# Kernel optimization log

Measured on AMD Instinct MI355X. Metric: run time of the kernel, lower is better.

The kernel has to match this reference:

```python
import jax, jax.numpy as jnp
import numpy as np
import math

IN_CH = 256
CH = 128
SCALE = math.sqrt(CH)
TEMPERATURE = 1.0


def setup_inputs() -> dict:
    key = jax.random.key(0)
    ks = jax.random.split(key, 9)
    B, C, H, W = 8, IN_CH, 56, 56
    x = jax.random.normal(ks[0], (B, C, H, W), dtype=jnp.float32)
    s_in = 1.0 / math.sqrt(IN_CH)
    s_ch = 1.0 / math.sqrt(CH)
    wq = jax.random.uniform(ks[1], (CH, IN_CH), minval=-s_in, maxval=s_in)
    bq = jax.random.uniform(ks[2], (CH,), minval=-s_in, maxval=s_in)
    wk = jax.random.uniform(ks[3], (CH, IN_CH), minval=-s_in, maxval=s_in)
    bk = jax.random.uniform(ks[4], (CH,), minval=-s_in, maxval=s_in)
    wv = jax.random.uniform(ks[5], (CH, IN_CH), minval=-s_in, maxval=s_in)
    bv = jax.random.uniform(ks[6], (CH,), minval=-s_in, maxval=s_in)
    wo = jax.random.uniform(ks[7], (IN_CH, CH), minval=-s_ch, maxval=s_ch)
    bo = jax.random.uniform(ks[8], (IN_CH,), minval=-s_ch, maxval=s_ch)
    return {"x": x, "wq": wq, "bq": bq, "wk": wk, "bk": bk,
            "wv": wv, "bv": bv, "wo": wo, "bo": bo}


def reference(x, wq, bq, wk, bk, wv, bv, wo, bo):
    B, C, H, W = x.shape
    N = H * W
    xf = x.reshape(B, C, N)  # flatten spatial; 1x1 conv == channel matmul
    q = jnp.einsum('oc,bcn->bon', wq, xf) + bq[None, :, None]  # (B,CH,N)
    k = jnp.einsum('oc,bcn->bon', wk, xf) + bk[None, :, None]
    v = jnp.einsum('oc,bcn->bon', wv, xf) + bv[None, :, None]
    # similarity map (B, N, N): query positions x key positions
    sim = jnp.einsum('bcn,bcm->bnm', q, k) / (SCALE * TEMPERATURE)
    attn = jax.nn.softmax(sim, axis=2)
    out = jnp.einsum('bnm,bcm->bnc', attn, v)  # (B, N, CH)
    out = jnp.einsum('oc,bnc->bon', wo, out) + bo[None, :, None]  # (B,IN_CH,N)
    return x + out.reshape(B, C, H, W)
```

## Files before the change

kernel.cpp:

```cpp
#include <hip/hip_runtime.h>
#include <hip/hip_bf16.h>
#include <math.h>

#define NPOS 3136
#define NB   8
#define LOG2E 1.44269504088896f
#define QSCALE (0.08838834764831845f * LOG2E)
#define OFS2  11.54156032711168f

typedef __attribute__((ext_vector_type(8))) short shortx8;
typedef __attribute__((ext_vector_type(4))) short shortx4;
typedef __attribute__((ext_vector_type(4))) float f32x4;
typedef __attribute__((ext_vector_type(16))) float f32x16;
typedef __attribute__((ext_vector_type(4))) unsigned int uint4v;

struct S8pair { shortx4 lo, hi; };

__device__ __forceinline__ float bf2f(unsigned short u) {
    unsigned int i = ((unsigned int)u) << 16;
    return __builtin_bit_cast(float, i);
}
__device__ __forceinline__ unsigned short f2bf(float f) {
    unsigned int i = __builtin_bit_cast(unsigned int, f);
    i += 0x7FFFu + ((i >> 16) & 1u);
    return (unsigned short)(i >> 16);
}
__device__ __forceinline__ void gll16(const unsigned short* g, unsigned short* l) {
    __builtin_amdgcn_global_load_lds((const __attribute__((address_space(1))) void*)g,
                                     (__attribute__((address_space(3))) void*)l, 16, 0, 0);
}

__global__ __launch_bounds__(256) void cast_w(
    const float* __restrict__ wq, const float* __restrict__ wk,
    const float* __restrict__ wv, const float* __restrict__ wo,
    unsigned short* __restrict__ Wb)
{
    const int sel = blockIdx.y;
    const float* src = (sel == 0) ? wq : (sel == 1) ? wk : (sel == 2) ? wv : wo;
    const float sc = (sel == 0) ? QSCALE : 1.0f;
    unsigned short* dst = Wb + sel * 32768;
    int i0 = (blockIdx.x * 256 + threadIdx.x) * 8;
    #pragma unroll
    for (int e = 0; e < 8; ++e) dst[i0 + e] = f2bf(src[i0 + e] * sc);
}

__global__ __launch_bounds__(256) void cast_xT(
    const float* __restrict__ x, unsigned short* __restrict__ xT)
{
    const int b = blockIdx.z, c0 = blockIdx.y * 64, n0 = blockIdx.x * 64;
    __shared__ unsigned short Ls[64 * 66];
    const int t = threadIdx.x;
    {
        int r = t >> 2, q4 = t & 3;
        const float* src = x + ((size_t)b * 256 + c0 + r) * NPOS + n0 + q4 * 16;
        #pragma unroll
        for (int i = 0; i < 16; ++i) Ls[r * 66 + q4 * 16 + i] = f2bf(src[i]);
    }
    __syncthreads();
    {
        int j = t >> 2, h4 = t & 3;
        shortx8 v0, v1;
        #pragma unroll
        for (int i = 0; i < 8; ++i) v0[i] = (short)Ls[(h4 * 16 + i) * 66 + j];
        #pragma unroll
        for (int i = 0; i < 8; ++i) v1[i] = (short)Ls[(h4 * 16 + 8 + i) * 66 + j];
        unsigned short* dst = xT + ((size_t)b * NPOS + n0 + j) * 256 + c0 + h4 * 16;
        *reinterpret_cast<shortx8*>(dst) = v0;
        *reinterpret_cast<shortx8*>(dst + 8) = v1;
    }
}

__global__ __launch_bounds__(256) void qkv_mfma(
    const unsigned short* __restrict__ xT,
    const unsigned short* __restrict__ Wb,
    const float* __restrict__ bq, const float* __restrict__ bk, const float* __restrict__ bv,
    unsigned short* __restrict__ qT, unsigned short* __restrict__ kT,
    unsigned short* __restrict__ vC)
{
    const int b = blockIdx.z, sel = blockIdx.y, n0 = blockIdx.x * 64;
    const int t = threadIdx.x, lane = t & 63, wave = t >> 6;
    const int l16 = lane & 15, lhi = lane >> 4;
    __shared__ __align__(16) unsigned short Wt[128 * 128];
    __shared__ __align__(16) unsigned short Xt[64 * 128];
    const unsigned short* Wsel = Wb + sel * 32768;
    const float* bias = (sel == 0) ? bq : (sel == 1) ? bk : bv;

    f32x4 acc[2][4];
    #pragma unroll
    for (int ab = 0; ab < 2; ++ab)
        #pragma unroll
        for (int nb = 0; nb < 4; ++nb) acc[ab][nb] = f32x4{0.f, 0.f, 0.f, 0.f};

    for (int ks0 = 0; ks0 < 2; ++ks0) {
        const int k0 = ks0 * 128;
        __syncthreads();
        #pragma unroll
        for (int i = 0; i < 8; ++i) {
            int c = (wave * 8 + i) * 64 + lane;
            int row = c >> 4, cin = (c & 15) ^ (row & 7);
            gll16(Wsel + (size_t)row * 256 + k0 + cin * 8, &Wt[0] + (wave * 8 + i) * 512);
        }
        #pragma unroll
        for (int i = 0; i < 4; ++i) {
            int c = (wave * 4 + i) * 64 + lane;
            int row = c >> 4, cin = (c & 15) ^ (row & 7);
            gll16(xT + ((size_t)b * NPOS + n0 + row) * 256 + k0 + cin * 8,
                  &Xt[0] + (wave * 4 + i) * 512);
        }
        __syncthreads();
        #pragma unroll
        for (int ks = 0; ks < 4; ++ks) {
            shortx8 aW[2];
            #pragma unroll
            for (int ab = 0; ab < 2; ++ab) {
                int row = wave * 32 + ab * 16 + l16;
                int idx = (row * 128 + ks * 32 + lhi * 8) ^ ((row & 7) << 3);
                aW[ab] = *reinterpret_cast<const shortx8*>(Wt + idx);
            }
            #pragma unroll
            for (int nb = 0; nb < 4; ++nb) {
                int row = nb * 16 + l16;
                int idx = (row * 128 + ks * 32 + lhi * 8) ^ ((row & 7) << 3);
                shortx8 bX = *reinterpret_cast<const shortx8*>(Xt + idx);
                acc[0][nb] = __builtin_amdgcn_mfma_f32_16x16x32_bf16(aW[0], bX, acc[0][nb], 0, 0, 0);
                acc[1][nb] = __builtin_amdgcn_mfma_f32_16x16x32_bf16(aW[1], bX, acc[1][nb], 0, 0, 0);
            }
        }
    }
    const int strip = wave * 32;
    if (sel < 2) {
        unsigned short* dst0 = ((sel == 0) ? qT : kT) + (size_t)b * NPOS * 128;
        const float bsc = (sel == 0) ? QSCALE : 1.0f;
        #pragma unroll
        for (int ab = 0; ab < 2; ++ab) {
            int ocb = strip + ab * 16 + lhi * 4;
            float bb[4];
            #pragma unroll
            for (int j = 0; j < 4; ++j) bb[j] = bias[ocb + j] * bsc;
            #pragma unroll
            for (int nb = 0; nb < 4; ++nb) {
                int n = n0 + nb * 16 + l16;
                shortx4 u;
                #pragma unroll
                for (int j = 0; j < 4; ++j) u[j] = (short)f2bf(acc[ab][nb][j] + bb[j]);
                *reinterpret_cast<shortx4*>(dst0 + (size_t)n * 128 + ocb) = u;
            }
        }
    } else {
        #pragma unroll
        for (int ab = 0; ab < 2; ++ab)
            #pragma unroll
            for (int j = 0; j < 4; ++j) {
                int oc = strip + ab * 16 + lhi * 4 + j;
                float bb = bias[oc];
                unsigned short* dst = vC + ((size_t)b * 128 + oc) * NPOS + n0;
                #pragma unroll
                for (int nb = 0; nb < 4; ++nb)
                    dst[nb * 16 + l16] = f2bf(acc[ab][nb][j] + bb);
            }
    }
}

__global__ __launch_bounds__(256) void attn_kernel(
    const unsigned short* __restrict__ qT,
    const unsigned short* __restrict__ kT,
    const unsigned short* __restrict__ vC,
    unsigned short* __restrict__ ao,
    float* __restrict__ lrG)
{
    const int i_lin = blockIdx.y * 49 + blockIdx.x;
    const int b = i_lin & 7;
    const int n0 = (i_lin >> 3) * 64;
    const int t = threadIdx.x, lane = t & 63, wave = t >> 6;
    const int l31 = lane & 31, h = lane >> 5;
    const int qsub = wave >> 1, kh = wave & 1;
    const int NT = NPOS / 64;

    __shared__ __align__(16) unsigned short KsB[2][64 * 128];
    __shared__ __align__(16) unsigned short VsB[2][128 * 64];

    shortx8 aQ[8];
    {
        const unsigned short* qp = qT + ((size_t)b * NPOS + n0 + qsub * 32 + l31) * 128 + h * 8;
        #pragma unroll
        for (int kk = 0; kk < 8; ++kk)
            aQ[kk] = *reinterpret_cast<const shortx8*>(qp + kk * 16);
    }

    const unsigned short* kSrc[4];
    const unsigned short* vSrc[4];
    unsigned sDst[4];
    #pragma unroll
    for (int i = 0; i < 4; ++i) {
        int c = (wave * 4 + i) * 64 + lane;
        int rK = c >> 4, cK = (c & 15) ^ (rK & 15);
        kSrc[i] = kT + ((size_t)b * NPOS + rK) * 128 + cK * 8;
        int rV = c >> 3, cV = (c & 7) ^ (rV & 7);
        vSrc[i] = vC + ((size_t)b * 128 + rV) * NPOS + cV * 8;
        sDst[i] = (wave * 4 + i) * 512;
    }

    unsigned kIdx[8];
    {
        int rowK = kh * 32 + l31;
        #pragma unroll
        for (int kk = 0; kk < 8; ++kk)
            kIdx[kk] = rowK * 128 + (((kk * 2 + h) ^ (rowK & 15)) * 8);
    }
    unsigned vBase[4], vM8[4];
    #pragma unroll
    for (int ob = 0; ob < 4; ++ob) {
        int rowV = ob * 32 + l31;
        vBase[ob] = rowV * 64 + h * 4;
        vM8[ob] = (rowV & 7) * 8;
    }

    f32x16 o[4];
    #pragma unroll
    for (int ob = 0; ob < 4; ++ob)
        #pragma unroll
        for (int r = 0; r < 16; ++r) o[ob][r] = 0.f;
    float lrP = 0.f;

    #define STAGE(kt_, buf_)                                                          \
        _Pragma("unroll")                                                             \
        for (int i = 0; i < 4; ++i) {                                                 \
            gll16(kSrc[i] + (size_t)(kt_) * 8192, &KsB[buf_][0] + sDst[i]);           \
            gll16(vSrc[i] + (kt_) * 64, &VsB[buf_][0] + sDst[i]);                     \
        }

    #define COMPUTE(Ks, Vs)                                                           \
    {                                                                                 \
        f32x16 sA, sB;                                                                \
        _Pragma("unroll")                                                             \
        for (int r = 0; r < 16; ++r) { sA[r] = 0.f; sB[r] = 0.f; }                    \
        __builtin_amdgcn_s_setprio(1);                                                \
        _Pragma("unroll")                                                             \
        for (int kk = 0; kk < 8; kk += 2) {                                           \
            shortx8 k0 = *reinterpret_cast<const shortx8*>((Ks) + kIdx[kk]);          \
            shortx8 k1 = *reinterpret_cast<const shortx8*>((Ks) + kIdx[kk + 1]);      \
            sA = __builtin_amdgcn_mfma_f32_32x32x16_bf16(k0, aQ[kk], sA, 0, 0, 0);    \
            sB = __builtin_amdgcn_mfma_f32_32x32x16_bf16(k1, aQ[kk + 1], sB, 0, 0, 0);\
        }                                                                             \
        __builtin_amdgcn_s_setprio(0);                                                \
        unsigned pk[8];                                                               \
        _Pragma("unroll")                                                             \
        for (int g = 0; g < 4; ++g) {                                                 \
            float p0 = exp2f(sA[g * 4 + 0] + sB[g * 4 + 0] - OFS2);                   \
            float p1 = exp2f(sA[g * 4 + 1] + sB[g * 4 + 1] - OFS2);                   \
            float p2 = exp2f(sA[g * 4 + 2] + sB[g * 4 + 2] - OFS2);                   \
            float p3 = exp2f(sA[g * 4 + 3] + sB[g * 4 + 3] - OFS2);                   \
            lrP += (p0 + p1) + (p2 + p3);                                             \
            asm("v_cvt_pk_bf16_f32 %0, %1, %2" : "=v"(pk[g * 2 + 0]) : "v"(p0), "v"(p1)); \
            asm("v_cvt_pk_bf16_f32 %0, %1, %2" : "=v"(pk[g * 2 + 1]) : "v"(p2), "v"(p3)); \
        }                                                                             \
        __builtin_amdgcn_s_setprio(1);                                                \
        _Pragma("unroll")                                                             \
        for (int ks = 0; ks < 2; ++ks) {                                              \
            uint4v pv = {pk[ks * 4 + 0], pk[ks * 4 + 1], pk[ks * 4 + 2], pk[ks * 4 + 3]}; \
            shortx8 PA = __builtin_bit_cast(shortx8, pv);                             \
            _Pragma("unroll")                                                         \
            for (int ob = 0; ob < 4; ++ob) {                                          \
                unsigned i0 = vBase[ob] + (((kh * 4 + ks * 2 + 0) * 8) ^ vM8[ob]);    \
                unsigned i1 = vBase[ob] + (((kh * 4 + ks * 2 + 1) * 8) ^ vM8[ob]);    \
                shortx4 lo = *reinterpret_cast<const shortx4*>((Vs) + i0);            \
                shortx4 hi = *reinterpret_cast<const shortx4*>((Vs) + i1);            \
                shortx8 bV = __builtin_bit_cast(shortx8, S8pair{lo, hi});             \
                o[ob] = __builtin_amdgcn_mfma_f32_32x32x16_bf16(PA, bV, o[ob], 0, 0, 0); \
            }                                                                         \
        }                                                                             \
        __builtin_amdgcn_s_setprio(0);                                                \
    }

    STAGE(0, 0)
    STAGE(1, 1)

    int cur = 0;
    for (int kt = 0; kt < NT - 1; ++kt) {
        asm volatile("s_waitcnt vmcnt(8)" ::: "memory");
        __builtin_amdgcn_sched_barrier(0);
        __builtin_amdgcn_s_barrier();
        __builtin_amdgcn_sched_barrier(0);
        COMPUTE(&KsB[cur][0], &VsB[cur][0])
        __builtin_amdgcn_sched_barrier(0);
        __builtin_amdgcn_s_barrier();
        __builtin_amdgcn_sched_barrier(0);
        if (kt < NT - 2) { STAGE(kt + 2, cur) }
        cur ^= 1;
    }
    {
        asm volatile("s_waitcnt vmcnt(0)" ::: "memory");
        __builtin_amdgcn_sched_barrier(0);
        __builtin_amdgcn_s_barrier();
        COMPUTE(&KsB[cur][0], &VsB[cur][0])
    }
    __syncthreads();

    float lr2 = lrP + __shfl_xor(lrP, 32);
    float* Om = reinterpret_cast<float*>(&KsB[0][0]);
    float* lrS = reinterpret_cast<float*>(&VsB[1][0]);
    unsigned short* Oo = &VsB[0][0];

    if (kh == 1) {
        #pragma unroll
        for (int ob = 0; ob < 4; ++ob)
            #pragma unroll
            for (int r = 0; r < 16; ++r) {
                int q = qsub * 32 + (r & 3) + 8 * (r >> 2) + 4 * h;
                Om[q * 128 + ob * 32 + l31] = o[ob][r];
            }
        if (lane < 32) lrS[qsub * 32 + l31] = lr2;
    }
    __syncthreads();
    if (kh == 0) {
        #pragma unroll
        for (int ob = 0; ob < 4; ++ob)
            #pragma unroll
            for (int r = 0; r < 16; ++r) {
                int q = qsub * 32 + (r & 3) + 8 * (r >> 2) + 4 * h;
                int idx = q * 128 + ob * 32 + l31;
                Oo[idx] = f2bf(o[ob][r] + Om[idx]);
            }
        if (lane < 32)
            lrG[(size_t)b * NPOS + n0 + qsub * 32 + l31] = lr2 + lrS[qsub * 32 + l31];
    }
    __syncthreads();
    {
        const shortx8* src = reinterpret_cast<const shortx8*>(Oo);
        shortx8* dst = reinterpret_cast<shortx8*>(ao + ((size_t)b * NPOS + n0) * 128);
        #pragma unroll
        for (int i = 0; i < 4; ++i) dst[t + 256 * i] = src[t + 256 * i];
    }
    #undef STAGE
    #undef COMPUTE
}

__global__ __launch_bounds__(256) void out_proj(
    const float* __restrict__ x,
    const unsigned short* __restrict__ Wb,
    const float* __restrict__ bo,
    const unsigned short* __restrict__ ao,
    const float* __restrict__ lrG,
    float* __restrict__ y)
{
    const int b = blockIdx.y, n0 = blockIdx.x * 64;
    const int t = threadIdx.x, lane = t & 63, wave = t >> 6;
    const int l16 = lane & 15, lhi = lane >> 4;
    __shared__ __align__(16) unsigned short Wt[256 * 128];
    __shared__ __align__(16) unsigned short At[64 * 128];
    const unsigned short* wo = Wb + 98304;

    #pragma unroll
    for (int i = 0; i < 16; ++i) {
        int c = (wave * 16 + i) * 64 + lane;
        int row = c >> 4, cin = (c & 15) ^ (row & 7);
        gll16(wo + (size_t)row * 128 + cin * 8, &Wt[0] + (wave * 16 + i) * 512);
    }
    #pragma unroll
    for (int i = 0; i < 4; ++i) {
        int c = (wave * 4 + i) * 64 + lane;
        int row = c >> 4, cin = (c & 15) ^ (row & 7);
        gll16(ao + ((size_t)b * NPOS + n0 + row) * 128 + cin * 8, &At[0] + (wave * 4 + i) * 512);
    }
    __syncthreads();

    f32x4 acc[4][4];
    #pragma unroll
    for (int ab = 0; ab < 4; ++ab)
        #pragma unroll
        for (int nb = 0; nb < 4; ++nb) acc[ab][nb] = f32x4{0.f, 0.f, 0.f, 0.f};

    const int strip = wave * 64;
    #pragma unroll
    for (int ks = 0; ks < 4; ++ks) {
        shortx8 aW[4];
        #pragma unroll
        for (int ab = 0; ab < 4; ++ab) {
            int row = strip + ab * 16 + l16;
            int idx = (row * 128 + ks * 32 + lhi * 8) ^ ((row & 7) << 3);
            aW[ab] = *reinterpret_cast<const shortx8*>(Wt + idx);
        }
        #pragma unroll
        for (int nb = 0; nb < 4; ++nb) {
            int row = nb * 16 + l16;
            int idx = (row * 128 + ks * 32 + lhi * 8) ^ ((row & 7) << 3);
            shortx8 bA = *reinterpret_cast<const shortx8*>(At + idx);
            #pragma unroll
            for (int ab = 0; ab < 4; ++ab)
                acc[ab][nb] = __builtin_amdgcn_mfma_f32_16x16x32_bf16(aW[ab], bA, acc[ab][nb], 0, 0, 0);
        }
    }

    float inv[4];
    #pragma unroll
    for (int nb = 0; nb < 4; ++nb)
        inv[nb] = 1.0f / lrG[(size_t)b * NPOS + n0 + nb * 16 + l16];

    #pragma unroll
    for (int ab = 0; ab < 4; ++ab)
        #pragma unroll
        for (int j = 0; j < 4; ++j) {
            int oc = strip + ab * 16 + lhi * 4 + j;
            float bb = bo[oc];
            const float* xr = x + ((size_t)b * 256 + oc) * NPOS + n0;
            float* yr = y + ((size_t)b * 256 + oc) * NPOS + n0;
            #pragma unroll
            for (int nb = 0; nb < 4; ++nb) {
                int n = nb * 16 + l16;
                yr[n] = xr[n] + bb + acc[ab][nb][j] * inv[nb];
            }
        }
}

extern "C" void kernel_launch(void* const* d_in, const int* in_sizes, int n_in,
                              void* d_out, int out_size, void* d_ws, size_t ws_size,
                              hipStream_t stream)
{
    const float* x  = (const float*)d_in[0];
    const float* wq = (const float*)d_in[1];
    const float* bq = (const float*)d_in[2];
    const float* wk = (const float*)d_in[3];
    const float* bk = (const float*)d_in[4];
    const float* wv = (const float*)d_in[5];
    const float* bv = (const float*)d_in[6];
    const float* wo = (const float*)d_in[7];
    const float* bo = (const float*)d_in[8];
    float* y = (float*)d_out;

    const size_t sz = (size_t)NB * NPOS * 128;
    unsigned short* qT = (unsigned short*)d_ws;
    unsigned short* kT = qT + sz;
    unsigned short* vC = kT + sz;
    unsigned short* xT = vC + sz;
    unsigned short* ao = xT;
    unsigned short* Wb = xT + 2 * sz;
    float* lrG = (float*)(Wb + 131072);

    cast_w  <<<dim3(16, 4),       256, 0, stream>>>(wq, wk, wv, wo, Wb);
    cast_xT <<<dim3(49, 4, NB),   256, 0, stream>>>(x, xT);
    qkv_mfma<<<dim3(49, 3, NB),   256, 0, stream>>>(xT, Wb, bq, bk, bv, qT, kT, vC);
    attn_kernel<<<dim3(49, NB),   256, 0, stream>>>(qT, kT, vC, ao, lrG);
    out_proj<<<dim3(49, NB),      256, 0, stream>>>(x, Wb, bo, ao, lrG, y);
}
```

Measured before the change: 122.2 us.

## Split attention key range across two blocks and merge partials in out_proj

The attention kernel now launches twice as many blocks, and each one covers half of the 49 key tiles (25 and 24). Each block writes an unnormalized partial output and a partial row sum to separate slices of the workspace, which the output projection sums before dividing. The aim is to fill the GPU's compute units better, since 392 blocks on 256 CUs leaves the machine unevenly loaded, and 784 smaller blocks balance it. The cost is extra traffic for the partial outputs and double the A-operand loads and MFMAs in out_proj. It relies on the fixed exponent offset rather than a running max, so the partials can be added without rescaling. V LDS indices are also precomputed into registers.

```diff
diff --git a/kernel.cpp b/kernel.cpp
--- a/kernel.cpp
+++ b/kernel.cpp
@@ -168,13 +168,15 @@
     unsigned short* __restrict__ ao,
     float* __restrict__ lrG)
 {
-    const int i_lin = blockIdx.y * 49 + blockIdx.x;
-    const int b = i_lin & 7;
-    const int n0 = (i_lin >> 3) * 64;
+    const int id = blockIdx.x + 49 * blockIdx.y + 392 * blockIdx.z;
+    const int b = id & 7;
+    const int r = id >> 3;
+    const int z = (r >= 49) ? 1 : 0;
+    const int n0 = (z ? r - 49 : r) * 64;
+    const int kt0 = z ? 25 : 0, kt1 = z ? 49 : 25;
     const int t = threadIdx.x, lane = t & 63, wave = t >> 6;
     const int l31 = lane & 31, h = lane >> 5;
     const int qsub = wave >> 1, kh = wave & 1;
-    const int NT = NPOS / 64;
 
     __shared__ __align__(16) unsigned short KsB[2][64 * 128];
     __shared__ __align__(16) unsigned short VsB[2][128 * 64];
@@ -207,19 +209,23 @@
         for (int kk = 0; kk < 8; ++kk)
             kIdx[kk] = rowK * 128 + (((kk * 2 + h) ^ (rowK & 15)) * 8);
     }
-    unsigned vBase[4], vM8[4];
+    unsigned vIdx[4][2][2];
     #pragma unroll
     for (int ob = 0; ob < 4; ++ob) {
         int rowV = ob * 32 + l31;
-        vBase[ob] = rowV * 64 + h * 4;
-        vM8[ob] = (rowV & 7) * 8;
+        #pragma unroll
+        for (int ks = 0; ks < 2; ++ks)
+            #pragma unroll
+            for (int rr = 0; rr < 2; ++rr)
+                vIdx[ob][ks][rr] = rowV * 64 + h * 4
+                    + (((kh * 4 + ks * 2 + rr) * 8) ^ ((rowV & 7) * 8));
     }
 
     f32x16 o[4];
     #pragma unroll
     for (int ob = 0; ob < 4; ++ob)
         #pragma unroll
-        for (int r = 0; r < 16; ++r) o[ob][r] = 0.f;
+        for (int r2 = 0; r2 < 16; ++r2) o[ob][r2] = 0.f;
     float lrP = 0.f;
 
     #define STAGE(kt_, buf_)                                                          \
@@ -233,7 +239,7 @@
     {                                                                                 \
         f32x16 sA, sB;                                                                \
         _Pragma("unroll")                                                             \
-        for (int r = 0; r < 16; ++r) { sA[r] = 0.f; sB[r] = 0.f; }                    \
+        for (int r2 = 0; r2 < 16; ++r2) { sA[r2] = 0.f; sB[r2] = 0.f; }               \
         __builtin_amdgcn_s_setprio(1);                                                \
         _Pragma("unroll")                                                             \
         for (int kk = 0; kk < 8; kk += 2) {                                           \
@@ -261,10 +267,8 @@
             shortx8 PA = __builtin_bit_cast(shortx8, pv);                             \
             _Pragma("unroll")                                                         \
             for (int ob = 0; ob < 4; ++ob) {                                          \
-                unsigned i0 = vBase[ob] + (((kh * 4 + ks * 2 + 0) * 8) ^ vM8[ob]);    \
-                unsigned i1 = vBase[ob] + (((kh * 4 + ks * 2 + 1) * 8) ^ vM8[ob]);    \
-                shortx4 lo = *reinterpret_cast<const shortx4*>((Vs) + i0);            \
-                shortx4 hi = *reinterpret_cast<const shortx4*>((Vs) + i1);            \
+                shortx4 lo = *reinterpret_cast<const shortx4*>((Vs) + vIdx[ob][ks][0]); \
+                shortx4 hi = *reinterpret_cast<const shortx4*>((Vs) + vIdx[ob][ks][1]); \
                 shortx8 bV = __builtin_bit_cast(shortx8, S8pair{lo, hi});             \
                 o[ob] = __builtin_amdgcn_mfma_f32_32x32x16_bf16(PA, bV, o[ob], 0, 0, 0); \
             }                                                                         \
@@ -272,11 +276,11 @@
         __builtin_amdgcn_s_setprio(0);                                                \
     }
 
-    STAGE(0, 0)
-    STAGE(1, 1)
+    STAGE(kt0, 0)
+    STAGE(kt0 + 1, 1)
 
     int cur = 0;
-    for (int kt = 0; kt < NT - 1; ++kt) {
+    for (int kt = kt0; kt < kt1 - 1; ++kt) {
         asm volatile("s_waitcnt vmcnt(8)" ::: "memory");
         __builtin_amdgcn_sched_barrier(0);
         __builtin_amdgcn_s_barrier();
@@ -285,7 +289,7 @@
         __builtin_amdgcn_sched_barrier(0);
         __builtin_amdgcn_s_barrier();
         __builtin_amdgcn_sched_barrier(0);
-        if (kt < NT - 2) { STAGE(kt + 2, cur) }
+        if (kt < kt1 - 2) { STAGE(kt + 2, cur) }
         cur ^= 1;
     }
     {
@@ -305,9 +309,9 @@
         #pragma unroll
         for (int ob = 0; ob < 4; ++ob)
             #pragma unroll
-            for (int r = 0; r < 16; ++r) {
-                int q = qsub * 32 + (r & 3) + 8 * (r >> 2) + 4 * h;
-                Om[q * 128 + ob * 32 + l31] = o[ob][r];
+            for (int r2 = 0; r2 < 16; ++r2) {
+                int q = qsub * 32 + (r2 & 3) + 8 * (r2 >> 2) + 4 * h;
+                Om[q * 128 + ob * 32 + l31] = o[ob][r2];
             }
         if (lane < 32) lrS[qsub * 32 + l31] = lr2;
     }
@@ -316,18 +320,20 @@
         #pragma unroll
         for (int ob = 0; ob < 4; ++ob)
             #pragma unroll
-            for (int r = 0; r < 16; ++r) {
-                int q = qsub * 32 + (r & 3) + 8 * (r >> 2) + 4 * h;
+            for (int r2 = 0; r2 < 16; ++r2) {
+                int q = qsub * 32 + (r2 & 3) + 8 * (r2 >> 2) + 4 * h;
                 int idx = q * 128 + ob * 32 + l31;
-                Oo[idx] = f2bf(o[ob][r] + Om[idx]);
+                Oo[idx] = f2bf(o[ob][r2] + Om[idx]);
             }
         if (lane < 32)
-            lrG[(size_t)b * NPOS + n0 + qsub * 32 + l31] = lr2 + lrS[qsub * 32 + l31];
+            lrG[((size_t)z * NB + b) * NPOS + n0 + qsub * 32 + l31]
+                = lr2 + lrS[qsub * 32 + l31];
     }
     __syncthreads();
     {
         const shortx8* src = reinterpret_cast<const shortx8*>(Oo);
-        shortx8* dst = reinterpret_cast<shortx8*>(ao + ((size_t)b * NPOS + n0) * 128);
+        shortx8* dst = reinterpret_cast<shortx8*>(
+            ao + (((size_t)z * NB + b) * NPOS + n0) * 128);
         #pragma unroll
         for (int i = 0; i < 4; ++i) dst[t + 256 * i] = src[t + 256 * i];
     }
@@ -347,7 +353,7 @@
     const int t = threadIdx.x, lane = t & 63, wave = t >> 6;
     const int l16 = lane & 15, lhi = lane >> 4;
     __shared__ __align__(16) unsigned short Wt[256 * 128];
-    __shared__ __align__(16) unsigned short At[64 * 128];
+    __shared__ __align__(16) unsigned short At[2][64 * 128];
     const unsigned short* wo = Wb + 98304;
 
     #pragma unroll
@@ -357,11 +363,14 @@
         gll16(wo + (size_t)row * 128 + cin * 8, &Wt[0] + (wave * 16 + i) * 512);
     }
     #pragma unroll
-    for (int i = 0; i < 4; ++i) {
-        int c = (wave * 4 + i) * 64 + lane;
-        int row = c >> 4, cin = (c & 15) ^ (row & 7);
-        gll16(ao + ((size_t)b * NPOS + n0 + row) * 128 + cin * 8, &At[0] + (wave * 4 + i) * 512);
-    }
+    for (int zz = 0; zz < 2; ++zz)
+        #pragma unroll
+        for (int i = 0; i < 4; ++i) {
+            int c = (wave * 4 + i) * 64 + lane;
+            int row = c >> 4, cin = (c & 15) ^ (row & 7);
+            gll16(ao + (((size_t)zz * NB + b) * NPOS + n0 + row) * 128 + cin * 8,
+                  &At[zz][0] + (wave * 4 + i) * 512);
+        }
     __syncthreads();
 
     f32x4 acc[4][4];
@@ -384,17 +393,22 @@
         for (int nb = 0; nb < 4; ++nb) {
             int row = nb * 16 + l16;
             int idx = (row * 128 + ks * 32 + lhi * 8) ^ ((row & 7) << 3);
-            shortx8 bA = *reinterpret_cast<const shortx8*>(At + idx);
-            #pragma unroll
-            for (int ab = 0; ab < 4; ++ab)
-                acc[ab][nb] = __builtin_amdgcn_mfma_f32_16x16x32_bf16(aW[ab], bA, acc[ab][nb], 0, 0, 0);
+            shortx8 bA0 = *reinterpret_cast<const shortx8*>(&At[0][0] + idx);
+            shortx8 bA1 = *reinterpret_cast<const shortx8*>(&At[1][0] + idx);
+            #pragma unroll
+            for (int ab = 0; ab < 4; ++ab) {
+                acc[ab][nb] = __builtin_amdgcn_mfma_f32_16x16x32_bf16(aW[ab], bA0, acc[ab][nb], 0, 0, 0);
+                acc[ab][nb] = __builtin_amdgcn_mfma_f32_16x16x32_bf16(aW[ab], bA1, acc[ab][nb], 0, 0, 0);
+            }
         }
     }
 
     float inv[4];
     #pragma unroll
-    for (int nb = 0; nb < 4; ++nb)
-        inv[nb] = 1.0f / lrG[(size_t)b * NPOS + n0 + nb * 16 + l16];
+    for (int nb = 0; nb < 4; ++nb) {
+        size_t n = (size_t)b * NPOS + n0 + nb * 16 + l16;
+        inv[nb] = 1.0f / (lrG[n] + lrG[(size_t)NB * NPOS + n]);
+    }
 
     #pragma unroll
     for (int ab = 0; ab < 4; ++ab)
@@ -436,9 +450,9 @@
     unsigned short* Wb = xT + 2 * sz;
     float* lrG = (float*)(Wb + 131072);
 
-    cast_w  <<<dim3(16, 4),       256, 0, stream>>>(wq, wk, wv, wo, Wb);
-    cast_xT <<<dim3(49, 4, NB),   256, 0, stream>>>(x, xT);
-    qkv_mfma<<<dim3(49, 3, NB),   256, 0, stream>>>(xT, Wb, bq, bk, bv, qT, kT, vC);
-    attn_kernel<<<dim3(49, NB),   256, 0, stream>>>(qT, kT, vC, ao, lrG);
-    out_proj<<<dim3(49, NB),      256, 0, stream>>>(x, Wb, bo, ao, lrG, y);
-}
+    cast_w  <<<dim3(16, 4),        256, 0, stream>>>(wq, wk, wv, wo, Wb);
+    cast_xT <<<dim3(49, 4, NB),    256, 0, stream>>>(x, xT);
+    qkv_mfma<<<dim3(49, 3, NB),    256, 0, stream>>>(xT, Wb, bq, bk, bv, qT, kT, vC);
+    attn_kernel<<<dim3(49, NB, 2), 256, 0, stream>>>(qT, kT, vC, ao, lrG);
+    out_proj<<<dim3(49, NB),       256, 0, stream>>>(x, Wb, bo, ao, lrG, y);
+}
```

New measurement: 136.6 us. 11.8% more time.
